# Kernel optimization log

Measured on AMD Instinct MI355X. Metric: run time of the kernel, lower is better.

Reference implementation:

```python
import jax, jax.numpy as jnp
import numpy as np

C = 1024
H = 16
DH = C // H
T = 2048
B = 2
EPS = 1e-5


def setup_inputs() -> dict:
    key = jax.random.key(0)
    ks = jax.random.split(key, 11)
    s = 1.0 / np.sqrt(C)
    return {
        "x": jax.random.normal(ks[0], (B, C, T), dtype=jnp.float32),
        "Wq": jax.random.normal(ks[1], (C, C), dtype=jnp.float32) * s,
        "bq": jax.random.normal(ks[2], (C,), dtype=jnp.float32) * 0.01,
        "Wk": jax.random.normal(ks[3], (C, C), dtype=jnp.float32) * s,
        "bk": jax.random.normal(ks[4], (C,), dtype=jnp.float32) * 0.01,
        "Wv": jax.random.normal(ks[5], (C, C), dtype=jnp.float32) * s,
        "bv": jax.random.normal(ks[6], (C,), dtype=jnp.float32) * 0.01,
        "Wo": jax.random.normal(ks[7], (C, C), dtype=jnp.float32) * s,
        "bo": jax.random.normal(ks[8], (C,), dtype=jnp.float32) * 0.01,
        "gamma": jax.random.normal(ks[9], (C,), dtype=jnp.float32) * 0.1,
        "beta": jax.random.normal(ks[10], (C,), dtype=jnp.float32) * 0.1,
    }


def reference(x, Wq, bq, Wk, bk, Wv, bv, Wo, bo, gamma, beta):
    scale = DH ** (-0.5)
    # conv1x1 projections: [B,C,T] x [C_out,C_in] -> [B,C,T]
    q = jnp.einsum('bct,dc->bdt', x, Wq) + bq[None, :, None]
    k = jnp.einsum('bct,dc->bdt', x, Wk) + bk[None, :, None]
    v = jnp.einsum('bct,dc->bdt', x, Wv) + bv[None, :, None]
    # split heads: [B,C,T] -> [B,H,Dh,T]
    q = q.reshape(B, H, DH, T).transpose(0, 1, 3, 2) * scale  # [B,H,T,Dh]
    k = k.reshape(B, H, DH, T)                                # [B,H,Dh,T]
    v = v.reshape(B, H, DH, T).transpose(0, 1, 3, 2)          # [B,H,T,Dh]
    sim = jnp.einsum('bhtd,bhds->bhts', q, k)                 # [B,H,T,T]
    attn = jax.nn.softmax(sim, axis=-1)
    attn = jnp.nan_to_num(attn, nan=0.0)
    out = jnp.einsum('bhts,bhsd->bhtd', attn, v)              # [B,H,T,Dh]
    out = out.transpose(0, 1, 3, 2).reshape(B, C, T)          # [B,C,T]
    y = jnp.einsum('bct,dc->bdt', out, Wo) + bo[None, :, None]
    # BatchNorm1d (training mode: batch statistics over B and T)
    mean = jnp.mean(y, axis=(0, 2), keepdims=True)
    var = jnp.var(y, axis=(0, 2), keepdims=True)
    y = (y - mean) * jax.lax.rsqrt(var + EPS)
    y = y * gamma[None, :, None] + beta[None, :, None]
    return x + y
```

## Files before the change

### kernel.cpp

```cpp
#include <hip/hip_runtime.h>

#define CC 1024
#define HH 16
#define DHH 64
#define TT 2048
#define BB 2

typedef short s8v __attribute__((ext_vector_type(8)));
typedef float f32x4 __attribute__((ext_vector_type(4)));

__device__ __forceinline__ unsigned short f2bf(float f) {
    union { float f; unsigned int u; } v; v.f = f;
    unsigned int r = v.u + 0x7FFFu + ((v.u >> 16) & 1u);
    return (unsigned short)(r >> 16);
}

__device__ __forceinline__ float fexp2(float x) {
#if __has_builtin(__builtin_amdgcn_exp2f)
    return __builtin_amdgcn_exp2f(x);
#else
    return exp2f(x);
#endif
}

__device__ __forceinline__ void gl_lds16(const unsigned short* g, unsigned short* l) {
    __builtin_amdgcn_global_load_lds(
        (const __attribute__((address_space(1))) unsigned int*)g,
        (__attribute__((address_space(3))) unsigned int*)l, 16, 0, 0);
}

__device__ __forceinline__ s8v lds_ld(const unsigned short* base, int byteoff) {
    return *(const s8v*)((const char*)base + byteoff);
}

__device__ __forceinline__ int xcd_swz(int orig, int nwg) {
    int cpx = nwg >> 3;
    return (orig & 7) * cpx + (orig >> 3);
}

__global__ void transpose_cast(const float* __restrict__ x, unsigned short* __restrict__ xT) {
    __shared__ float tile[32][33];
    int b = blockIdx.z;
    int t0 = blockIdx.x * 32, c0 = blockIdx.y * 32;
    int tx = threadIdx.x, ty = threadIdx.y;
    const float* xb = x + (size_t)b * CC * TT;
    #pragma unroll
    for (int i = 0; i < 32; i += 8)
        tile[ty + i][tx] = xb[(size_t)(c0 + ty + i) * TT + t0 + tx];
    __syncthreads();
    unsigned short* xTb = xT + (size_t)b * TT * CC;
    #pragma unroll
    for (int i = 0; i < 32; i += 8)
        xTb[(size_t)(t0 + ty + i) * CC + c0 + tx] = f2bf(tile[tx][ty + i]);
}

__global__ void cast_weights(const float* __restrict__ Wq, const float* __restrict__ Wk,
                             const float* __restrict__ Wv, const float* __restrict__ Wo,
                             unsigned short* __restrict__ out) {
    int i = blockIdx.x * 256 + threadIdx.x;
    int which = i >> 18;
    int j = (i & 0x3FFFF) * 4;
    const float* s = (which == 0) ? Wq : (which == 1) ? Wk : (which == 2) ? Wv : Wo;
    float4 v = *(const float4*)(s + j);
    unsigned short* d = out + (size_t)which * 1048576 + j;
    ushort4 pk; pk.x = f2bf(v.x); pk.y = f2bf(v.y); pk.z = f2bf(v.z); pk.w = f2bf(v.w);
    *(ushort4*)d = pk;
}

template<int NFRAG>
__device__ __forceinline__ void gemm_core_k1024(
    const unsigned short* __restrict__ A, const unsigned short* __restrict__ Bt,
    unsigned short* As, unsigned short* Bs,
    int m0, int n0, int tid, f32x4 (&acc)[4][NFRAG]) {
    const int w = tid >> 6, l = tid & 63;
    const int ln = l & 15, hi = l >> 4;
    const int wm = (w >> 1) * 64, wn = (w & 1) * (NFRAG * 16);
    const int BSZ = NFRAG * 1024;
    int offA[4], offB[NFRAG];
    #pragma unroll
    for (int i = 0; i < 4; ++i) {
        int ra = wm + 16 * i + ln;
        offA[i] = ra * 64 + ((hi ^ ((ra >> 1) & 3)) * 16);
    }
    #pragma unroll
    for (int j = 0; j < NFRAG; ++j) {
        int rb = wn + 16 * j + ln;
        offB[j] = rb * 64 + ((hi ^ ((rb >> 1) & 3)) * 16);
    }
    const unsigned short* ap[2];
    const unsigned short* bp[NFRAG / 2];
    #pragma unroll
    for (int j = 0; j < 2; ++j) {
        int p = j * 256 + tid;
        int r = p >> 2, g = (p & 3) ^ ((r >> 1) & 3);
        ap[j] = A + (size_t)(m0 + r) * CC + 8 * g;
    }
    #pragma unroll
    for (int j = 0; j < NFRAG / 2; ++j) {
        int p = j * 256 + tid;
        int r = p >> 2, g = (p & 3) ^ ((r >> 1) & 3);
        bp[j] = Bt + (size_t)(n0 + r) * CC + 8 * g;
    }
    auto stage = [&](int buf) {
        #pragma unroll
        for (int j = 0; j < 2; ++j) {
            gl_lds16(ap[j], As + buf * 4096 + (j * 256 + w * 64) * 8);
            ap[j] += 32;
        }
        #pragma unroll
        for (int j = 0; j < NFRAG / 2; ++j) {
            gl_lds16(bp[j], Bs + buf * BSZ + (j * 256 + w * 64) * 8);
            bp[j] += 32;
        }
    };
    stage(0); stage(1); stage(2);
    if constexpr (NFRAG == 4) asm volatile("s_waitcnt vmcnt(8)" ::: "memory");
    else                      asm volatile("s_waitcnt vmcnt(6)" ::: "memory");
    __builtin_amdgcn_sched_barrier(0);
    __builtin_amdgcn_s_barrier();
    __builtin_amdgcn_sched_barrier(0);
    int buf = 0;
    for (int kk = 0; kk < 32; ++kk) {
        const unsigned short* Ab = As + buf * 4096;
        const unsigned short* Bb = Bs + buf * BSZ;
        s8v a[4], bb[NFRAG];
        #pragma unroll
        for (int i = 0; i < 4; ++i) a[i] = lds_ld(Ab, offA[i]);
        #pragma unroll
        for (int j = 0; j < NFRAG; ++j) bb[j] = lds_ld(Bb, offB[j]);
        __builtin_amdgcn_s_setprio(1);
        #pragma unroll
        for (int i = 0; i < 4; ++i)
            #pragma unroll
            for (int jj = 0; jj < NFRAG; ++jj)
                acc[i][jj] = __builtin_amdgcn_mfma_f32_16x16x32_bf16(a[i], bb[jj], acc[i][jj], 0, 0, 0);
        __builtin_amdgcn_s_setprio(0);
        if (kk < 31) {
            if (kk < 29) {
                if constexpr (NFRAG == 4) asm volatile("s_waitcnt vmcnt(4)" ::: "memory");
                else                      asm volatile("s_waitcnt vmcnt(3)" ::: "memory");
            } else {
                asm volatile("s_waitcnt vmcnt(0)" ::: "memory");
            }
            __builtin_amdgcn_sched_barrier(0);
            __builtin_amdgcn_s_barrier();
            __builtin_amdgcn_sched_barrier(0);
            if (kk < 29) stage(buf);
            buf = (buf == 2) ? 0 : buf + 1;
        }
    }
}

__global__ __launch_bounds__(256, 3)
void gemm_qkv(const unsigned short* __restrict__ xT, const unsigned short* __restrict__ Wb,
              unsigned short* __restrict__ qTp, unsigned short* __restrict__ kTp,
              unsigned short* __restrict__ vp,
              const float* __restrict__ bq, const float* __restrict__ bk,
              const float* __restrict__ bv, float qscale) {
    __shared__ unsigned short As[3 * 4096];
    __shared__ unsigned short Bs[3 * 4096];
    const int tid = threadIdx.x;
    const int wgid = xcd_swz(blockIdx.x, 768);
    const int z = wgid >> 7, bx = wgid & 127;
    const int which = z >> 1, b = z & 1;
    const long TC = (long)TT * CC;

    const unsigned short* A; const unsigned short* Bt;
    int m0, n0;
    if (which < 2) {
        A = xT + (size_t)b * TC;
        Bt = Wb + (size_t)which * 1048576;
        n0 = (bx & 7) * 128; m0 = (bx >> 3) * 128;
    } else {
        A = Wb + 2097152;
        Bt = xT + (size_t)b * TC;
        n0 = (bx & 15) * 128; m0 = (bx >> 4) * 128;
    }

    f32x4 acc[4][4] = {};
    gemm_core_k1024<4>(A, Bt, As, Bs, m0, n0, tid, acc);

    const int w = tid >> 6, l = tid & 63;
    const int ln = l & 15, hi = l >> 4;
    const int wm = (w >> 1) * 64, wn = (w & 1) * 64;

    if (which < 2) {
        unsigned short* Out = (which == 0 ? qTp : kTp) + (size_t)b * TC;
        const float* bias = (which == 0) ? bq : bk;
        float scale = (which == 0) ? qscale : 1.0f;
        #pragma unroll
        for (int i = 0; i < 4; ++i)
            #pragma unroll
            for (int jj = 0; jj < 4; ++jj) {
                int col = n0 + wn + 16 * jj + ln;
                float bvv = bias[col];
                #pragma unroll
                for (int r = 0; r < 4; ++r) {
                    int row = m0 + wm + 16 * i + hi * 4 + r;
                    Out[(size_t)row * CC + col] = f2bf((acc[i][jj][r] + bvv) * scale);
                }
            }
    } else {
        unsigned short* Out = vp + (size_t)b * TC;
        #pragma unroll
        for (int i = 0; i < 4; ++i)
            #pragma unroll
            for (int r = 0; r < 4; ++r) {
                int row = m0 + wm + 16 * i + hi * 4 + r;
                float bvv = bv[row];
                #pragma unroll
                for (int jj = 0; jj < 4; ++jj) {
                    int col = n0 + wn + 16 * jj + ln;
                    Out[(size_t)row * TT + col] = f2bf(acc[i][jj][r] + bvv);
                }
            }
    }
}

__global__ __launch_bounds__(256, 2)
void gemm_y(const unsigned short* __restrict__ Wo, const unsigned short* __restrict__ outT,
            float* __restrict__ y, const float* __restrict__ bo) {
    __shared__ unsigned short As[3 * 4096];
    __shared__ unsigned short Bs[3 * 2048];
    const int tid = threadIdx.x;
    const int wgid = xcd_swz(blockIdx.x, 512);
    const int b = wgid >> 8, bx = wgid & 255;
    const int n0 = (bx & 31) * 64, m0 = (bx >> 5) * 128;
    const long TC = (long)TT * CC;

    f32x4 acc[4][2] = {};
    gemm_core_k1024<2>(Wo, outT + (size_t)b * TC, As, Bs, m0, n0, tid, acc);

    const int w = tid >> 6, l = tid & 63;
    const int ln = l & 15, hi = l >> 4;
    const int wm = (w >> 1) * 64, wn = (w & 1) * 32;
    float* Out = y + (size_t)b * TC;
    #pragma unroll
    for (int i = 0; i < 4; ++i)
        #pragma unroll
        for (int r = 0; r < 4; ++r) {
            int row = m0 + wm + 16 * i + hi * 4 + r;
            float bvv = bo[row];
            #pragma unroll
            for (int jj = 0; jj < 2; ++jj) {
                int col = n0 + wn + 16 * jj + ln;
                Out[(size_t)row * TT + col] = acc[i][jj][r] + bvv;
            }
        }
}

__global__ __launch_bounds__(512, 4)
void attn_kernel(const unsigned short* __restrict__ qT,
                 const unsigned short* __restrict__ kT,
                 const unsigned short* __restrict__ vv,
                 unsigned short* __restrict__ oT) {
    __shared__ unsigned short Ks[2][128 * 64];
    __shared__ unsigned short Vs[2][64 * 128];

    const int tid = threadIdx.x;
    const int w = tid >> 6, l = tid & 63;
    const int ln = l & 15, hi = l >> 4;
    const int wgid = xcd_swz(blockIdx.x, 512);
    const int qt0 = (wgid & 15) * 128;
    const int bh = wgid >> 4;
    const int b = bh >> 4, h = bh & 15;
    const size_t bTT = (size_t)b * TT;

    const unsigned short* kp[2];
    const unsigned short* vp2[2];
    #pragma unroll
    for (int j = 0; j < 2; ++j) {
        int c = j * 512 + tid;
        int rk = c >> 3, gk = (c & 7) ^ (rk & 7);
        kp[j] = kT + (bTT + rk) * CC + h * DHH + 8 * gk;
        int rv = c >> 4, gv = (c & 15) ^ (rv & 7);
        vp2[j] = vv + ((size_t)b * CC + h * DHH + rv) * TT + 8 * gv;
    }
    auto stage = [&](int buf) {
        #pragma unroll
        for (int j = 0; j < 2; ++j)
            gl_lds16(kp[j], &Ks[buf][(j * 512 + w * 64) * 8]);
        #pragma unroll
        for (int j = 0; j < 2; ++j)
            gl_lds16(vp2[j], &Vs[buf][(j * 512 + w * 64) * 8]);
        #pragma unroll
        for (int j = 0; j < 2; ++j) { kp[j] += 128 * CC; vp2[j] += 128; }
    };

    stage(0);
    stage(1);

    s8v qf[2];
    {
        const unsigned short* qbase = qT + (bTT + qt0 + w * 16 + ln) * CC + h * DHH;
        #pragma unroll
        for (int kc = 0; kc < 2; ++kc)
            qf[kc] = *(const s8v*)(qbase + kc * 32 + 8 * hi);
    }

    int koff[8][2];
    #pragma unroll
    for (int cf = 0; cf < 8; ++cf) {
        int rk = cf * 16 + ln;
        koff[cf][0] = rk * 128 + ((hi ^ (rk & 7)) * 16);
        koff[cf][1] = rk * 128 + (((4 + hi) ^ (rk & 7)) * 16);
    }
    int voff[4][4];
    #pragma unroll
    for (int kc = 0; kc < 4; ++kc)
        #pragma unroll
        for (int nf = 0; nf < 4; ++nf) {
            int rv = nf * 16 + ln;
            voff[kc][nf] = rv * 256 + (((kc * 4 + hi) ^ (rv & 7)) * 16);
        }

    f32x4 of[4] = {};
    f32x4 sf[8];
    float li = 0.f;
    int fidx[4];
    #pragma unroll
    for (int r = 0; r < 4; ++r) fidx[r] = (l & 48) | (hi * 4 + r);

    asm volatile("s_waitcnt vmcnt(4)" ::: "memory");
    __builtin_amdgcn_sched_barrier(0);
    __builtin_amdgcn_s_barrier();
    __builtin_amdgcn_sched_barrier(0);

    auto qk = [&](int buf) {
        const unsigned short* Kb = &Ks[buf][0];
        #pragma unroll
        for (int cf = 0; cf < 8; ++cf) {
            s8v k0 = lds_ld(Kb, koff[cf][0]);
            s8v k1 = lds_ld(Kb, koff[cf][1]);
            __builtin_amdgcn_s_setprio(1);
            f32x4 t = (f32x4){0.f, 0.f, 0.f, 0.f};
            t = __builtin_amdgcn_mfma_f32_16x16x32_bf16(k0, qf[0], t, 0, 0, 0);
            t = __builtin_amdgcn_mfma_f32_16x16x32_bf16(k1, qf[1], t, 0, 0, 0);
            sf[cf] = t;
            __builtin_amdgcn_s_setprio(0);
        }
    };

    qk(0);

    unsigned int pw[8][2];
    for (int ti = 0; ti < 16; ++ti) {
        {
            float ps0 = 0.f, ps1 = 0.f, ps2 = 0.f, ps3 = 0.f;
            #pragma unroll
            for (int cf = 0; cf < 8; ++cf) {
                float p0 = fexp2(sf[cf][0]);
                float p1 = fexp2(sf[cf][1]);
                float p2 = fexp2(sf[cf][2]);
                float p3 = fexp2(sf[cf][3]);
                ps0 += p0; ps1 += p1; ps2 += p2; ps3 += p3;
                unsigned int w0, w1;
                asm("v_cvt_pk_bf16_f32 %0, %1, %2" : "=v"(w0) : "v"(p0), "v"(p1));
                asm("v_cvt_pk_bf16_f32 %0, %1, %2" : "=v"(w1) : "v"(p2), "v"(p3));
                pw[cf][0] = w0;
                pw[cf][1] = w1;
            }
            float ps = (ps0 + ps1) + (ps2 + ps3);
            ps += __shfl_xor(ps, 16);
            ps += __shfl_xor(ps, 32);
            li += ps;
        }

        {
            const unsigned short* Vb = &Vs[ti & 1][0];
            #pragma unroll
            for (int kc = 0; kc < 4; ++kc) {
                s8v pa;
                {
                    unsigned int A0 = pw[2 * kc][0], B0 = pw[2 * kc + 1][0];
                    unsigned int A1 = pw[2 * kc][1], B1 = pw[2 * kc + 1][1];
                    asm("v_permlane32_swap_b32 %0, %1" : "+v"(A0), "+v"(B0));
                    asm("v_permlane16_swap_b32 %0, %1" : "+v"(A0), "+v"(B0));
                    asm("v_permlane32_swap_b32 %0, %1" : "+v"(A1), "+v"(B1));
                    asm("v_permlane16_swap_b32 %0, %1" : "+v"(A1), "+v"(B1));
                    union { unsigned int u[4]; s8v v; } up;
                    up.u[0] = A0; up.u[1] = A1; up.u[2] = B0; up.u[3] = B1;
                    pa = up.v;
                }
                __builtin_amdgcn_s_setprio(1);
                #pragma unroll
                for (int nf = 0; nf < 4; ++nf) {
                    s8v vb = lds_ld(Vb, voff[kc][nf]);
                    of[nf] = __builtin_amdgcn_mfma_f32_16x16x32_bf16(pa, vb, of[nf], 0, 0, 0);
                }
                __builtin_amdgcn_s_setprio(0);
            }
        }

        if (ti < 15) {
            asm volatile("s_waitcnt vmcnt(0)" ::: "memory");
            __builtin_amdgcn_sched_barrier(0);
            __builtin_amdgcn_s_barrier();
            __builtin_amdgcn_sched_barrier(0);
            if (ti < 14) stage(ti & 1);
            qk((ti + 1) & 1);
        }
    }

    {
        float inv = 1.0f / li;
        float invr[4];
        #pragma unroll
        for (int r = 0; r < 4; ++r) invr[r] = __shfl(inv, fidx[r]);
        #pragma unroll
        for (int nf = 0; nf < 4; ++nf)
            #pragma unroll
            for (int r = 0; r < 4; ++r) {
                int row = qt0 + w * 16 + hi * 4 + r;
                int col = h * DHH + nf * 16 + ln;
                oT[(bTT + row) * CC + col] = f2bf(of[nf][r] * invr[r]);
            }
    }
}

__global__ __launch_bounds__(256)
void bn_apply(const float* __restrict__ x, const float* __restrict__ y,
              const float* __restrict__ gamma, const float* __restrict__ beta,
              float* __restrict__ out) {
    const int c = blockIdx.x;
    const int tid = threadIdx.x;
    const float* y0 = y + (size_t)c * TT;
    const float* y1 = y + (size_t)(CC + c) * TT;

    float s = 0.f, ss = 0.f;
    for (int t = tid * 4; t < TT; t += 1024) {
        float4 a = *(const float4*)(y0 + t);
        float4 d = *(const float4*)(y1 + t);
        s  += (a.x + a.y) + (a.z + a.w) + (d.x + d.y) + (d.z + d.w);
        ss += (a.x * a.x + a.y * a.y) + (a.z * a.z + a.w * a.w)
            + (d.x * d.x + d.y * d.y) + (d.z * d.z + d.w * d.w);
    }
    #pragma unroll
    for (int m = 1; m < 64; m <<= 1) { s += __shfl_xor(s, m); ss += __shfl_xor(ss, m); }
    __shared__ float a1[4], a2[4];
    __shared__ float sMean, sRstd;
    int wv = tid >> 6;
    if ((tid & 63) == 0) { a1[wv] = s; a2[wv] = ss; }
    __syncthreads();
    if (tid == 0) {
        float S = a1[0] + a1[1] + a1[2] + a1[3];
        float SS = a2[0] + a2[1] + a2[2] + a2[3];
        const float inv_n = 1.0f / (BB * TT);
        float mu = S * inv_n;
        sMean = mu;
        sRstd = rsqrtf(SS * inv_n - mu * mu + 1e-5f);
    }
    __syncthreads();
    float a = gamma[c] * sRstd;
    float bb = beta[c] - sMean * a;

    const float* x0 = x + (size_t)c * TT;
    const float* x1 = x + (size_t)(CC + c) * TT;
    float* o0 = out + (size_t)c * TT;
    float* o1 = out + (size_t)(CC + c) * TT;
    for (int t = tid * 4; t < TT; t += 1024) {
        float4 xv = *(const float4*)(x0 + t);
        float4 yv = *(const float4*)(y0 + t);
        float4 o;
        o.x = xv.x + a * yv.x + bb; o.y = xv.y + a * yv.y + bb;
        o.z = xv.z + a * yv.z + bb; o.w = xv.w + a * yv.w + bb;
        *(float4*)(o0 + t) = o;
        xv = *(const float4*)(x1 + t);
        yv = *(const float4*)(y1 + t);
        o.x = xv.x + a * yv.x + bb; o.y = xv.y + a * yv.y + bb;
        o.z = xv.z + a * yv.z + bb; o.w = xv.w + a * yv.w + bb;
        *(float4*)(o1 + t) = o;
    }
}

extern "C" void kernel_launch(void* const* d_in, const int* in_sizes, int n_in,
                              void* d_out, int out_size, void* d_ws, size_t ws_size,
                              hipStream_t stream) {
    const float* x     = (const float*)d_in[0];
    const float* Wq    = (const float*)d_in[1];
    const float* bq    = (const float*)d_in[2];
    const float* Wk    = (const float*)d_in[3];
    const float* bk    = (const float*)d_in[4];
    const float* Wv    = (const float*)d_in[5];
    const float* bv    = (const float*)d_in[6];
    const float* Wo    = (const float*)d_in[7];
    const float* bo    = (const float*)d_in[8];
    const float* gamma = (const float*)d_in[9];
    const float* beta  = (const float*)d_in[10];
    float* out = (float*)d_out;

    char* ws = (char*)d_ws;
    unsigned short* buf0 = (unsigned short*)(ws);
    unsigned short* Wb   = (unsigned short*)(ws + 8388608);
    unsigned short* qTp  = (unsigned short*)(ws + 16777216);
    unsigned short* kTp  = (unsigned short*)(ws + 25165824);
    unsigned short* vp   = (unsigned short*)(ws + 33554432);
    float* yp            = (float*)(ws + 16777216);

    transpose_cast<<<dim3(TT / 32, CC / 32, BB), dim3(32, 8), 0, stream>>>(x, buf0);
    cast_weights<<<dim3(4096), dim3(256), 0, stream>>>(Wq, Wk, Wv, Wo, Wb);

    gemm_qkv<<<dim3(768), dim3(256), 0, stream>>>(
        buf0, Wb, qTp, kTp, vp, bq, bk, bv, 0.125f * 1.4426950408889634f);

    attn_kernel<<<dim3(512), dim3(512), 0, stream>>>(qTp, kTp, vp, buf0);

    gemm_y<<<dim3(512), dim3(256), 0, stream>>>(Wb + 3145728, buf0, yp, bo);

    bn_apply<<<dim3(CC), dim3(256), 0, stream>>>(x, yp, gamma, beta, out);
}
```

Measured before the change: 119.6 us.

## Switch attention kernel to 32x32x16 MFMA with 4 waves of 32 query rows

```diff
diff --git a/kernel.cpp b/kernel.cpp
--- a/kernel.cpp
+++ b/kernel.cpp
@@ -8,6 +8,7 @@
 
 typedef short s8v __attribute__((ext_vector_type(8)));
 typedef float f32x4 __attribute__((ext_vector_type(4)));
+typedef float f32x16 __attribute__((ext_vector_type(16)));
 
 __device__ __forceinline__ unsigned short f2bf(float f) {
     union { float f; unsigned int u; } v; v.f = f;
@@ -249,7 +250,7 @@
         }
 }
 
-__global__ __launch_bounds__(512, 4)
+__global__ __launch_bounds__(256, 2)
 void attn_kernel(const unsigned short* __restrict__ qT,
                  const unsigned short* __restrict__ kT,
                  const unsigned short* __restrict__ vv,
@@ -259,18 +260,18 @@
 
     const int tid = threadIdx.x;
     const int w = tid >> 6, l = tid & 63;
-    const int ln = l & 15, hi = l >> 4;
+    const int l31 = l & 31, h5 = l >> 5, l7 = l & 7;
     const int wgid = xcd_swz(blockIdx.x, 512);
     const int qt0 = (wgid & 15) * 128;
     const int bh = wgid >> 4;
     const int b = bh >> 4, h = bh & 15;
     const size_t bTT = (size_t)b * TT;
 
-    const unsigned short* kp[2];
-    const unsigned short* vp2[2];
-    #pragma unroll
-    for (int j = 0; j < 2; ++j) {
-        int c = j * 512 + tid;
+    const unsigned short* kp[4];
+    const unsigned short* vp2[4];
+    #pragma unroll
+    for (int j = 0; j < 4; ++j) {
+        int c = j * 256 + tid;
         int rk = c >> 3, gk = (c & 7) ^ (rk & 7);
         kp[j] = kT + (bTT + rk) * CC + h * DHH + 8 * gk;
         int rv = c >> 4, gv = (c & 15) ^ (rv & 7);
@@ -278,116 +279,100 @@
     }
     auto stage = [&](int buf) {
         #pragma unroll
-        for (int j = 0; j < 2; ++j)
-            gl_lds16(kp[j], &Ks[buf][(j * 512 + w * 64) * 8]);
-        #pragma unroll
-        for (int j = 0; j < 2; ++j)
-            gl_lds16(vp2[j], &Vs[buf][(j * 512 + w * 64) * 8]);
-        #pragma unroll
-        for (int j = 0; j < 2; ++j) { kp[j] += 128 * CC; vp2[j] += 128; }
+        for (int j = 0; j < 4; ++j)
+            gl_lds16(kp[j], &Ks[buf][(j * 256 + w * 64) * 8]);
+        #pragma unroll
+        for (int j = 0; j < 4; ++j)
+            gl_lds16(vp2[j], &Vs[buf][(j * 256 + w * 64) * 8]);
+        #pragma unroll
+        for (int j = 0; j < 4; ++j) { kp[j] += 128 * CC; vp2[j] += 128; }
     };
 
     stage(0);
     stage(1);
 
-    s8v qf[2];
+    s8v qf[4];
     {
-        const unsigned short* qbase = qT + (bTT + qt0 + w * 16 + ln) * CC + h * DHH;
-        #pragma unroll
-        for (int kc = 0; kc < 2; ++kc)
-            qf[kc] = *(const s8v*)(qbase + kc * 32 + 8 * hi);
-    }
-
-    int koff[8][2];
-    #pragma unroll
-    for (int cf = 0; cf < 8; ++cf) {
-        int rk = cf * 16 + ln;
-        koff[cf][0] = rk * 128 + ((hi ^ (rk & 7)) * 16);
-        koff[cf][1] = rk * 128 + (((4 + hi) ^ (rk & 7)) * 16);
-    }
-    int voff[4][4];
-    #pragma unroll
-    for (int kc = 0; kc < 4; ++kc)
-        #pragma unroll
-        for (int nf = 0; nf < 4; ++nf) {
-            int rv = nf * 16 + ln;
-            voff[kc][nf] = rv * 256 + (((kc * 4 + hi) ^ (rv & 7)) * 16);
-        }
-
-    f32x4 of[4] = {};
-    f32x4 sf[8];
+        const unsigned short* qbase = qT + (bTT + qt0 + w * 32 + l31) * CC + h * DHH + h5 * 8;
+        #pragma unroll
+        for (int kk = 0; kk < 4; ++kk)
+            qf[kk] = *(const s8v*)(qbase + kk * 16);
+    }
+
+    int choff[8];
+    #pragma unroll
+    for (int i = 0; i < 8; ++i) choff[i] = ((2 * i + h5) ^ l7) * 16;
+    int rkb[4], rvb[2];
+    #pragma unroll
+    for (int cb = 0; cb < 4; ++cb) rkb[cb] = (32 * cb + l31) * 128;
+    #pragma unroll
+    for (int db = 0; db < 2; ++db) rvb[db] = (32 * db + l31) * 256;
+
+    f32x16 sf[4];
+    f32x16 of[2] = {};
     float li = 0.f;
-    int fidx[4];
-    #pragma unroll
-    for (int r = 0; r < 4; ++r) fidx[r] = (l & 48) | (hi * 4 + r);
-
-    asm volatile("s_waitcnt vmcnt(4)" ::: "memory");
+
+    asm volatile("s_waitcnt vmcnt(8)" ::: "memory");
     __builtin_amdgcn_sched_barrier(0);
     __builtin_amdgcn_s_barrier();
     __builtin_amdgcn_sched_barrier(0);
 
     auto qk = [&](int buf) {
         const unsigned short* Kb = &Ks[buf][0];
-        #pragma unroll
-        for (int cf = 0; cf < 8; ++cf) {
-            s8v k0 = lds_ld(Kb, koff[cf][0]);
-            s8v k1 = lds_ld(Kb, koff[cf][1]);
-            __builtin_amdgcn_s_setprio(1);
-            f32x4 t = (f32x4){0.f, 0.f, 0.f, 0.f};
-            t = __builtin_amdgcn_mfma_f32_16x16x32_bf16(k0, qf[0], t, 0, 0, 0);
-            t = __builtin_amdgcn_mfma_f32_16x16x32_bf16(k1, qf[1], t, 0, 0, 0);
-            sf[cf] = t;
-            __builtin_amdgcn_s_setprio(0);
-        }
+        __builtin_amdgcn_s_setprio(1);
+        #pragma unroll
+        for (int cb = 0; cb < 4; ++cb) {
+            f32x16 t = {};
+            #pragma unroll
+            for (int kk = 0; kk < 4; ++kk) {
+                s8v kf = lds_ld(Kb, rkb[cb] + choff[kk]);
+                t = __builtin_amdgcn_mfma_f32_32x32x16_bf16(kf, qf[kk], t, 0, 0, 0);
+            }
+            sf[cb] = t;
+        }
+        __builtin_amdgcn_s_setprio(0);
     };
 
     qk(0);
 
-    unsigned int pw[8][2];
+    unsigned int pw[16][2];
     for (int ti = 0; ti < 16; ++ti) {
         {
-            float ps0 = 0.f, ps1 = 0.f, ps2 = 0.f, ps3 = 0.f;
-            #pragma unroll
-            for (int cf = 0; cf < 8; ++cf) {
-                float p0 = fexp2(sf[cf][0]);
-                float p1 = fexp2(sf[cf][1]);
-                float p2 = fexp2(sf[cf][2]);
-                float p3 = fexp2(sf[cf][3]);
-                ps0 += p0; ps1 += p1; ps2 += p2; ps3 += p3;
-                unsigned int w0, w1;
-                asm("v_cvt_pk_bf16_f32 %0, %1, %2" : "=v"(w0) : "v"(p0), "v"(p1));
-                asm("v_cvt_pk_bf16_f32 %0, %1, %2" : "=v"(w1) : "v"(p2), "v"(p3));
-                pw[cf][0] = w0;
-                pw[cf][1] = w1;
-            }
-            float ps = (ps0 + ps1) + (ps2 + ps3);
-            ps += __shfl_xor(ps, 16);
-            ps += __shfl_xor(ps, 32);
+            float ps = 0.f;
+            #pragma unroll
+            for (int cb = 0; cb < 4; ++cb)
+                #pragma unroll
+                for (int q3 = 0; q3 < 4; ++q3) {
+                    float p0 = fexp2(sf[cb][4 * q3 + 0]);
+                    float p1 = fexp2(sf[cb][4 * q3 + 1]);
+                    float p2 = fexp2(sf[cb][4 * q3 + 2]);
+                    float p3 = fexp2(sf[cb][4 * q3 + 3]);
+                    ps += (p0 + p1) + (p2 + p3);
+                    unsigned int w0, w1;
+                    asm("v_cvt_pk_bf16_f32 %0, %1, %2" : "=v"(w0) : "v"(p0), "v"(p1));
+                    asm("v_cvt_pk_bf16_f32 %0, %1, %2" : "=v"(w1) : "v"(p2), "v"(p3));
+                    pw[4 * cb + q3][0] = w0;
+                    pw[4 * cb + q3][1] = w1;
+                }
             li += ps;
         }
 
         {
             const unsigned short* Vb = &Vs[ti & 1][0];
             #pragma unroll
-            for (int kc = 0; kc < 4; ++kc) {
-                s8v pa;
-                {
-                    unsigned int A0 = pw[2 * kc][0], B0 = pw[2 * kc + 1][0];
-                    unsigned int A1 = pw[2 * kc][1], B1 = pw[2 * kc + 1][1];
-                    asm("v_permlane32_swap_b32 %0, %1" : "+v"(A0), "+v"(B0));
-                    asm("v_permlane16_swap_b32 %0, %1" : "+v"(A0), "+v"(B0));
-                    asm("v_permlane32_swap_b32 %0, %1" : "+v"(A1), "+v"(B1));
-                    asm("v_permlane16_swap_b32 %0, %1" : "+v"(A1), "+v"(B1));
-                    union { unsigned int u[4]; s8v v; } up;
-                    up.u[0] = A0; up.u[1] = A1; up.u[2] = B0; up.u[3] = B1;
-                    pa = up.v;
-                }
+            for (int ks = 0; ks < 8; ++ks) {
+                unsigned int X0 = pw[2 * ks][0], Y0 = pw[2 * ks + 1][0];
+                unsigned int X1 = pw[2 * ks][1], Y1 = pw[2 * ks + 1][1];
+                asm("v_permlane32_swap_b32 %0, %1" : "+v"(X0), "+v"(Y0));
+                asm("v_permlane32_swap_b32 %0, %1" : "+v"(X1), "+v"(Y1));
+                union { unsigned int u[4]; s8v v; } up;
+                up.u[0] = X0; up.u[1] = X1; up.u[2] = Y0; up.u[3] = Y1;
+                s8v pa = up.v;
+                s8v vb0 = lds_ld(Vb, rvb[0] + choff[ks]);
+                s8v vb1 = lds_ld(Vb, rvb[1] + choff[ks]);
                 __builtin_amdgcn_s_setprio(1);
-                #pragma unroll
-                for (int nf = 0; nf < 4; ++nf) {
-                    s8v vb = lds_ld(Vb, voff[kc][nf]);
-                    of[nf] = __builtin_amdgcn_mfma_f32_16x16x32_bf16(pa, vb, of[nf], 0, 0, 0);
-                }
+                of[0] = __builtin_amdgcn_mfma_f32_32x32x16_bf16(pa, vb0, of[0], 0, 0, 0);
+                of[1] = __builtin_amdgcn_mfma_f32_32x32x16_bf16(pa, vb1, of[1], 0, 0, 0);
                 __builtin_amdgcn_s_setprio(0);
             }
         }
@@ -402,20 +387,18 @@
         }
     }
 
-    {
-        float inv = 1.0f / li;
-        float invr[4];
-        #pragma unroll
-        for (int r = 0; r < 4; ++r) invr[r] = __shfl(inv, fidx[r]);
-        #pragma unroll
-        for (int nf = 0; nf < 4; ++nf)
-            #pragma unroll
-            for (int r = 0; r < 4; ++r) {
-                int row = qt0 + w * 16 + hi * 4 + r;
-                int col = h * DHH + nf * 16 + ln;
-                oT[(bTT + row) * CC + col] = f2bf(of[nf][r] * invr[r]);
-            }
-    }
+    li += __shfl_xor(li, 32);
+    float inv = 1.0f / li;
+    #pragma unroll
+    for (int q3 = 0; q3 < 4; ++q3)
+        #pragma unroll
+        for (int s = 0; s < 4; ++s) {
+            float iv = __shfl(inv, 8 * q3 + s + 4 * h5);
+            int row = qt0 + w * 32 + 8 * q3 + s + 4 * h5;
+            size_t base = (bTT + row) * CC + h * DHH + l31;
+            oT[base] = f2bf(of[0][4 * q3 + s] * iv);
+            oT[base + 32] = f2bf(of[1][4 * q3 + s] * iv);
+        }
 }
 
 __global__ __launch_bounds__(256)
@@ -503,7 +486,7 @@
     gemm_qkv<<<dim3(768), dim3(256), 0, stream>>>(
         buf0, Wb, qTp, kTp, vp, bq, bk, bv, 0.125f * 1.4426950408889634f);
 
-    attn_kernel<<<dim3(512), dim3(512), 0, stream>>>(qTp, kTp, vp, buf0);
+    attn_kernel<<<dim3(512), dim3(256), 0, stream>>>(qTp, kTp, vp, buf0);
 
     gemm_y<<<dim3(512), dim3(256), 0, stream>>>(Wb + 3145728, buf0, yp, bo);
 
```

Result: no change. 119.3 us (-0.3%).
